# Kernel tuning notes

Hardware: AMD Instinct MI355X
Metric: run time of the kernel (lower is better)

The kernel has to match this reference:

```python
import jax, jax.numpy as jnp
import numpy as np

TEMPERATURE = 0.2
EPS = 1e-10

def setup_inputs() -> dict:
    key = jax.random.key(0)
    x = jax.random.normal(key, (8, 1024, 64, 64), dtype=jnp.float32)
    return {"x": x}

def reference(x):
    B, C, H, W = x.shape
    xf = x.reshape(B, C, H * W)                      # [B, C, HW]
    dot = jnp.einsum('bcn,bdn->bcd', xf, xf) / TEMPERATURE  # [B, C, C]
    logits = jax.nn.softmax(dot, axis=-1)
    diag = jnp.diagonal(logits, axis1=-2, axis2=-1)  # [B, C]
    loss = -jnp.log(diag + EPS)
    return jnp.mean(loss)
```

## Files before the change

### kernel.cpp

```cpp
#include <hip/hip_runtime.h>
#include <hip/hip_bf16.h>

#define BATCH 8
#define CCH 1024
#define NHW 4096
#define SCALE 5.0f
#define ROWS (BATCH * CCH)

typedef unsigned short u16;
typedef __attribute__((ext_vector_type(8))) short short8;
typedef __attribute__((ext_vector_type(4))) float float4v;

__device__ __forceinline__ void async_load16(const void* gsrc, void* ldst) {
    __builtin_amdgcn_global_load_lds(
        (__attribute__((address_space(1))) void*)gsrc,
        (__attribute__((address_space(3))) void*)ldst,
        16, 0, 0);
}

__device__ __forceinline__ u16 f2bf(float f) {
    union { float f; unsigned int u; } c; c.f = f;
    unsigned int u = c.u;
    unsigned int r = u + 0x7FFFu + ((u >> 16) & 1u);
    return (u16)(r >> 16);
}

template <bool CONVERT>
__global__ __launch_bounds__(256) void prep_kernel(const float* __restrict__ x,
                                                   u16* __restrict__ xbf,
                                                   float* __restrict__ diag,
                                                   float* __restrict__ l_acc) {
    const int row = blockIdx.x;
    const int tid = threadIdx.x;
    const float* src = x + (size_t)row * NHW;
    float ssum = 0.f;
#pragma unroll
    for (int p = 0; p < 4; ++p) {
        const int idx = p * 1024 + tid * 4;
        float4 v = *(const float4*)(src + idx);
        ssum += v.x * v.x + v.y * v.y + v.z * v.z + v.w * v.w;
        if (CONVERT) {
            ushort4 o;
            o.x = f2bf(v.x); o.y = f2bf(v.y); o.z = f2bf(v.z); o.w = f2bf(v.w);
            *(ushort4*)(xbf + (size_t)row * NHW + idx) = o;
        }
    }
#pragma unroll
    for (int m = 1; m < 64; m <<= 1) ssum += __shfl_xor(ssum, m);
    __shared__ float red[4];
    if ((tid & 63) == 0) red[tid >> 6] = ssum;
    __syncthreads();
    if (tid == 0) {
        diag[row] = (red[0] + red[1] + red[2] + red[3]) * SCALE;
        l_acc[row] = 0.f;
    }
}

template <bool BF16SRC>
__global__ __launch_bounds__(256) void gram_kernel(const u16* __restrict__ Xbf,
                                                   const float* __restrict__ Xf,
                                                   const float* __restrict__ diag,
                                                   float* __restrict__ l_acc,
                                                   float* __restrict__ num) {
    __shared__ __align__(16) u16 As[8192];
    __shared__ __align__(16) u16 Bs[4096];

    const int bid = blockIdx.x;
    const int b = bid & 7;
    const int t = bid >> 3;

    int bi = 0;
#pragma unroll
    for (int i = 7; i >= 1; --i) {
        if (t >= i * (17 - i)) { bi = i; break; }
    }
    const int bj2 = 2 * bi + (t - bi * (17 - bi));

    const int tid  = threadIdx.x;
    const int lane = tid & 63;
    const int w    = tid >> 6;
    const int wm   = w >> 1;
    const int wn   = w & 1;

    const int st_r  = lane >> 3;
    const int st_kc = (lane & 7) ^ (st_r & 7);

    const u16*   pA  = nullptr; const u16*   pB  = nullptr;
    const float* pAf = nullptr; const float* pBf = nullptr;
    if (BF16SRC) {
        const u16* baseX = Xbf + (size_t)b * CCH * NHW;
        pA = baseX + (size_t)(bi * 128 + w * 32 + st_r) * NHW + st_kc * 8;
        pB = baseX + (size_t)(bj2 * 64 + w * 16 + st_r) * NHW + st_kc * 8;
    } else {
        const float* baseXf = Xf + (size_t)b * CCH * NHW;
        pAf = baseXf + (size_t)(bi * 128 + w * 32 + st_r) * NHW + st_kc * 8;
        pBf = baseXf + (size_t)(bj2 * 64 + w * 16 + st_r) * NHW + st_kc * 8;
    }

    float4v acc[4][2] = {};

    for (int K0 = 0; K0 < NHW; K0 += 64) {
        __syncthreads();
        if (BF16SRC) {
#pragma unroll
            for (int t8 = 0; t8 < 4; ++t8)
                async_load16(pA + (size_t)t8 * 8 * NHW,
                             As + (size_t)(w * 32 + t8 * 8) * 64);
#pragma unroll
            for (int t8 = 0; t8 < 2; ++t8)
                async_load16(pB + (size_t)t8 * 8 * NHW,
                             Bs + (size_t)(w * 16 + t8 * 8) * 64);
            pA += 64; pB += 64;
        } else {
#pragma unroll
            for (int t8 = 0; t8 < 4; ++t8) {
                const float* s = pAf + (size_t)t8 * 8 * NHW;
                float4 f0 = *(const float4*)(s);
                float4 f1 = *(const float4*)(s + 4);
                u16* d = As + (size_t)(w * 32 + t8 * 8 + st_r) * 64 + (lane & 7) * 8;
                d[0]=f2bf(f0.x); d[1]=f2bf(f0.y); d[2]=f2bf(f0.z); d[3]=f2bf(f0.w);
                d[4]=f2bf(f1.x); d[5]=f2bf(f1.y); d[6]=f2bf(f1.z); d[7]=f2bf(f1.w);
            }
#pragma unroll
            for (int t8 = 0; t8 < 2; ++t8) {
                const float* s = pBf + (size_t)t8 * 8 * NHW;
                float4 f0 = *(const float4*)(s);
                float4 f1 = *(const float4*)(s + 4);
                u16* d = Bs + (size_t)(w * 16 + t8 * 8 + st_r) * 64 + (lane & 7) * 8;
                d[0]=f2bf(f0.x); d[1]=f2bf(f0.y); d[2]=f2bf(f0.z); d[3]=f2bf(f0.w);
                d[4]=f2bf(f1.x); d[5]=f2bf(f1.y); d[6]=f2bf(f1.z); d[7]=f2bf(f1.w);
            }
            pAf += 64; pBf += 64;
        }
        __syncthreads();

#pragma unroll
        for (int ks = 0; ks < 2; ++ks) {
            short8 af[4], bf[2];
            const int kq = ks * 4 + (lane >> 4);
            const int rl = lane & 15;
            const int slot = kq ^ (rl & 7);
#pragma unroll
            for (int mt = 0; mt < 4; ++mt)
                af[mt] = *(const short8*)(As + (size_t)(wm * 64 + mt * 16 + rl) * 64 + slot * 8);
#pragma unroll
            for (int nt = 0; nt < 2; ++nt)
                bf[nt] = *(const short8*)(Bs + (size_t)(wn * 32 + nt * 16 + rl) * 64 + slot * 8);
#pragma unroll
            for (int mt = 0; mt < 4; ++mt)
#pragma unroll
                for (int nt = 0; nt < 2; ++nt)
                    acc[mt][nt] = __builtin_amdgcn_mfma_f32_16x16x32_bf16(af[mt], bf[nt], acc[mt][nt], 0, 0, 0);
        }
    }

    const int q  = lane >> 4;
    const int cl = lane & 15;
    const int rowbase = bi * 128 + wm * 64;
    const int colbase = bj2 * 64 + wn * 32;
    const float* dgb = diag + b * CCH;
    float* lb = l_acc + b * CCH;

#pragma unroll
    for (int mt = 0; mt < 4; ++mt) {
#pragma unroll
        for (int reg = 0; reg < 4; ++reg) {
            const int gr = rowbase + mt * 16 + q * 4 + reg;
            const float dg = dgb[gr];
            float s = 0.f;
#pragma unroll
            for (int nt = 0; nt < 2; ++nt) {
                const int gc = colbase + nt * 16 + cl;
                const float e = __expf(acc[mt][nt][reg] * SCALE - dg);
                if (gr <= gc) s += e;
                if (gr == gc) num[b * CCH + gr] = e;
            }
            s += __shfl_xor(s, 1);
            s += __shfl_xor(s, 2);
            s += __shfl_xor(s, 4);
            s += __shfl_xor(s, 8);
            if (cl == 0) atomicAdd(lb + gr, s);
        }
    }

#pragma unroll
    for (int nt = 0; nt < 2; ++nt) {
        const int gc = colbase + nt * 16 + cl;
        const float dgc = dgb[gc];
        float s = 0.f;
#pragma unroll
        for (int mt = 0; mt < 4; ++mt) {
#pragma unroll
            for (int reg = 0; reg < 4; ++reg) {
                const int gr = rowbase + mt * 16 + q * 4 + reg;
                if (gr < gc) s += __expf(acc[mt][nt][reg] * SCALE - dgc);
            }
        }
        s += __shfl_xor(s, 16);
        s += __shfl_xor(s, 32);
        if (lane < 16) atomicAdd(lb + gc, s);
    }
}

__global__ __launch_bounds__(1024) void finalize_kernel(const float* __restrict__ l_acc,
                                                        const float* __restrict__ num,
                                                        float* __restrict__ out) {
    const int tid = threadIdx.x;
    float s = 0.f;
    for (int r = tid; r < ROWS; r += 1024) {
        const float d = num[r] / l_acc[r];
        s += -__logf(d + 1e-10f);
    }
#pragma unroll
    for (int m = 1; m < 64; m <<= 1) s += __shfl_xor(s, m);
    __shared__ float red[16];
    if ((tid & 63) == 0) red[tid >> 6] = s;
    __syncthreads();
    if (tid == 0) {
        float tot = 0.f;
#pragma unroll
        for (int i = 0; i < 16; ++i) tot += red[i];
        out[0] = tot * (1.0f / (float)ROWS);
    }
}

extern "C" void kernel_launch(void* const* d_in, const int* in_sizes, int n_in,
                              void* d_out, int out_size, void* d_ws, size_t ws_size,
                              hipStream_t stream) {
    const float* x = (const float*)d_in[0];
    float* out = (float*)d_out;

    const size_t xbf_bytes  = (size_t)BATCH * CCH * NHW * 2;
    const size_t stat_bytes = (size_t)ROWS * 4;
    const bool fast = ws_size >= xbf_bytes + 3 * stat_bytes;

    const int ntiles = 72;

    if (fast) {
        u16*   xbf   = (u16*)d_ws;
        float* diag  = (float*)((char*)d_ws + xbf_bytes);
        float* l_acc = diag + ROWS;
        float* num   = l_acc + ROWS;
        prep_kernel<true><<<ROWS, 256, 0, stream>>>(x, xbf, diag, l_acc);
        gram_kernel<true><<<BATCH * ntiles, 256, 0, stream>>>(xbf, nullptr, diag, l_acc, num);
        finalize_kernel<<<1, 1024, 0, stream>>>(l_acc, num, out);
    } else {
        float* diag  = (float*)d_ws;
        float* l_acc = diag + ROWS;
        float* num   = l_acc + ROWS;
        prep_kernel<false><<<ROWS, 256, 0, stream>>>(x, nullptr, diag, l_acc);
        gram_kernel<false><<<BATCH * ntiles, 256, 0, stream>>>(nullptr, x, diag, l_acc, num);
        finalize_kernel<<<1, 1024, 0, stream>>>(l_acc, num, out);
    }
}
```

Baseline: 255.7 us.

## Switch Gram kernel to 64x64 upper-triangular tiles with K=128 steps

Replaces the 128x64 block tiling over the symmetric Gram matrix with 64x64 tiles covering the upper triangle (136 tiles per batch instead of 72). Diagonal tiles load only one operand and reuse it as both A and B. The K loop now steps by 128 with a reworked XOR swizzle for LDS. The aim is less wasted work on the diagonal and more blocks for better occupancy across CUs. The cost is lower per-block data reuse and more loads and atomics in total.

```diff
diff --git a/kernel.cpp b/kernel.cpp
--- a/kernel.cpp
+++ b/kernel.cpp
@@ -63,7 +63,7 @@
                                                    float* __restrict__ l_acc,
                                                    float* __restrict__ num) {
     __shared__ __align__(16) u16 As[8192];
-    __shared__ __align__(16) u16 Bs[4096];
+    __shared__ __align__(16) u16 Bs[8192];
 
     const int bid = blockIdx.x;
     const int b = bid & 7;
@@ -71,10 +71,11 @@
 
     int bi = 0;
 #pragma unroll
-    for (int i = 7; i >= 1; --i) {
-        if (t >= i * (17 - i)) { bi = i; break; }
-    }
-    const int bj2 = 2 * bi + (t - bi * (17 - bi));
+    for (int i = 15; i >= 1; --i) {
+        if (t >= i * 16 - (i * (i - 1)) / 2) { bi = i; break; }
+    }
+    const int bj = bi + (t - (bi * 16 - (bi * (bi - 1)) / 2));
+    const bool diagtile = (bi == bj);
 
     const int tid  = threadIdx.x;
     const int lane = tid & 63;
@@ -82,72 +83,82 @@
     const int wm   = w >> 1;
     const int wn   = w & 1;
 
-    const int st_r  = lane >> 3;
-    const int st_kc = (lane & 7) ^ (st_r & 7);
+    const int st_r4 = lane >> 4;
+    const int st_k0 = (lane & 15) ^ st_r4;
 
     const u16*   pA  = nullptr; const u16*   pB  = nullptr;
     const float* pAf = nullptr; const float* pBf = nullptr;
     if (BF16SRC) {
         const u16* baseX = Xbf + (size_t)b * CCH * NHW;
-        pA = baseX + (size_t)(bi * 128 + w * 32 + st_r) * NHW + st_kc * 8;
-        pB = baseX + (size_t)(bj2 * 64 + w * 16 + st_r) * NHW + st_kc * 8;
+        pA = baseX + (size_t)(bi * 64 + w * 16 + st_r4) * NHW;
+        pB = baseX + (size_t)(bj * 64 + w * 16 + st_r4) * NHW;
     } else {
         const float* baseXf = Xf + (size_t)b * CCH * NHW;
-        pAf = baseXf + (size_t)(bi * 128 + w * 32 + st_r) * NHW + st_kc * 8;
-        pBf = baseXf + (size_t)(bj2 * 64 + w * 16 + st_r) * NHW + st_kc * 8;
-    }
-
-    float4v acc[4][2] = {};
-
-    for (int K0 = 0; K0 < NHW; K0 += 64) {
+        pAf = baseXf + (size_t)(bi * 64 + w * 16 + st_r4) * NHW;
+        pBf = baseXf + (size_t)(bj * 64 + w * 16 + st_r4) * NHW;
+    }
+
+    float4v acc[2][2] = {};
+
+    for (int K0 = 0; K0 < NHW; K0 += 128) {
         __syncthreads();
         if (BF16SRC) {
 #pragma unroll
-            for (int t8 = 0; t8 < 4; ++t8)
-                async_load16(pA + (size_t)t8 * 8 * NHW,
-                             As + (size_t)(w * 32 + t8 * 8) * 64);
-#pragma unroll
-            for (int t8 = 0; t8 < 2; ++t8)
-                async_load16(pB + (size_t)t8 * 8 * NHW,
-                             Bs + (size_t)(w * 16 + t8 * 8) * 64);
-            pA += 64; pB += 64;
+            for (int t4 = 0; t4 < 4; ++t4) {
+                const int kc = st_k0 ^ (t4 * 4);
+                async_load16(pA + (size_t)(t4 * 4) * NHW + K0 + kc * 8,
+                             As + (size_t)(w * 16 + t4 * 4) * 128);
+            }
+            if (!diagtile) {
+#pragma unroll
+                for (int t4 = 0; t4 < 4; ++t4) {
+                    const int kc = st_k0 ^ (t4 * 4);
+                    async_load16(pB + (size_t)(t4 * 4) * NHW + K0 + kc * 8,
+                                 Bs + (size_t)(w * 16 + t4 * 4) * 128);
+                }
+            }
         } else {
 #pragma unroll
-            for (int t8 = 0; t8 < 4; ++t8) {
-                const float* s = pAf + (size_t)t8 * 8 * NHW;
+            for (int t4 = 0; t4 < 4; ++t4) {
+                const int kc = st_k0 ^ (t4 * 4);
+                const float* s = pAf + (size_t)(t4 * 4) * NHW + K0 + kc * 8;
                 float4 f0 = *(const float4*)(s);
                 float4 f1 = *(const float4*)(s + 4);
-                u16* d = As + (size_t)(w * 32 + t8 * 8 + st_r) * 64 + (lane & 7) * 8;
+                u16* d = As + (size_t)(w * 16 + t4 * 4 + st_r4) * 128 + (lane & 15) * 8;
                 d[0]=f2bf(f0.x); d[1]=f2bf(f0.y); d[2]=f2bf(f0.z); d[3]=f2bf(f0.w);
                 d[4]=f2bf(f1.x); d[5]=f2bf(f1.y); d[6]=f2bf(f1.z); d[7]=f2bf(f1.w);
             }
-#pragma unroll
-            for (int t8 = 0; t8 < 2; ++t8) {
-                const float* s = pBf + (size_t)t8 * 8 * NHW;
-                float4 f0 = *(const float4*)(s);
-                float4 f1 = *(const float4*)(s + 4);
-                u16* d = Bs + (size_t)(w * 16 + t8 * 8 + st_r) * 64 + (lane & 7) * 8;
-                d[0]=f2bf(f0.x); d[1]=f2bf(f0.y); d[2]=f2bf(f0.z); d[3]=f2bf(f0.w);
-                d[4]=f2bf(f1.x); d[5]=f2bf(f1.y); d[6]=f2bf(f1.z); d[7]=f2bf(f1.w);
-            }
-            pAf += 64; pBf += 64;
+            if (!diagtile) {
+#pragma unroll
+                for (int t4 = 0; t4 < 4; ++t4) {
+                    const int kc = st_k0 ^ (t4 * 4);
+                    const float* s = pBf + (size_t)(t4 * 4) * NHW + K0 + kc * 8;
+                    float4 f0 = *(const float4*)(s);
+                    float4 f1 = *(const float4*)(s + 4);
+                    u16* d = Bs + (size_t)(w * 16 + t4 * 4 + st_r4) * 128 + (lane & 15) * 8;
+                    d[0]=f2bf(f0.x); d[1]=f2bf(f0.y); d[2]=f2bf(f0.z); d[3]=f2bf(f0.w);
+                    d[4]=f2bf(f1.x); d[5]=f2bf(f1.y); d[6]=f2bf(f1.z); d[7]=f2bf(f1.w);
+                }
+            }
         }
         __syncthreads();
 
-#pragma unroll
-        for (int ks = 0; ks < 2; ++ks) {
-            short8 af[4], bf[2];
-            const int kq = ks * 4 + (lane >> 4);
+        const u16* Bbase = diagtile ? As : Bs;
+#pragma unroll
+        for (int ks = 0; ks < 4; ++ks) {
+            short8 af[2], bf[2];
+            const int q  = lane >> 4;
             const int rl = lane & 15;
-            const int slot = kq ^ (rl & 7);
-#pragma unroll
-            for (int mt = 0; mt < 4; ++mt)
-                af[mt] = *(const short8*)(As + (size_t)(wm * 64 + mt * 16 + rl) * 64 + slot * 8);
+            const int kq = ks * 4 + q;
+            const int slot = kq ^ rl;
+#pragma unroll
+            for (int mt = 0; mt < 2; ++mt)
+                af[mt] = *(const short8*)(As + (size_t)(wm * 32 + mt * 16 + rl) * 128 + slot * 8);
 #pragma unroll
             for (int nt = 0; nt < 2; ++nt)
-                bf[nt] = *(const short8*)(Bs + (size_t)(wn * 32 + nt * 16 + rl) * 64 + slot * 8);
-#pragma unroll
-            for (int mt = 0; mt < 4; ++mt)
+                bf[nt] = *(const short8*)(Bbase + (size_t)(wn * 32 + nt * 16 + rl) * 128 + slot * 8);
+#pragma unroll
+            for (int mt = 0; mt < 2; ++mt)
 #pragma unroll
                 for (int nt = 0; nt < 2; ++nt)
                     acc[mt][nt] = __builtin_amdgcn_mfma_f32_16x16x32_bf16(af[mt], bf[nt], acc[mt][nt], 0, 0, 0);
@@ -156,13 +167,13 @@
 
     const int q  = lane >> 4;
     const int cl = lane & 15;
-    const int rowbase = bi * 128 + wm * 64;
-    const int colbase = bj2 * 64 + wn * 32;
+    const int rowbase = bi * 64 + wm * 32;
+    const int colbase = bj * 64 + wn * 32;
     const float* dgb = diag + b * CCH;
     float* lb = l_acc + b * CCH;
 
 #pragma unroll
-    for (int mt = 0; mt < 4; ++mt) {
+    for (int mt = 0; mt < 2; ++mt) {
 #pragma unroll
         for (int reg = 0; reg < 4; ++reg) {
             const int gr = rowbase + mt * 16 + q * 4 + reg;
@@ -189,7 +200,7 @@
         const float dgc = dgb[gc];
         float s = 0.f;
 #pragma unroll
-        for (int mt = 0; mt < 4; ++mt) {
+        for (int mt = 0; mt < 2; ++mt) {
 #pragma unroll
             for (int reg = 0; reg < 4; ++reg) {
                 const int gr = rowbase + mt * 16 + q * 4 + reg;
@@ -234,7 +245,7 @@
     const size_t stat_bytes = (size_t)ROWS * 4;
     const bool fast = ws_size >= xbf_bytes + 3 * stat_bytes;
 
-    const int ntiles = 72;
+    const int ntiles = 136;
 
     if (fast) {
         u16*   xbf   = (u16*)d_ws;
```

Result: slower. 263.1 us (+2.9%).

## Switch Gram matrix path from bf16 to fp8 MFMA with diagonal tile aliasing

Applied to the files above, without the earlier changes.

Quantizes the input to fp8 instead of bf16 in the prep pass, halving the workspace footprint, and runs the Gram matrix on the fp8 16x16x32 MFMA with a K step of 128 per LDS stage. The diagonal is computed from the dequantized fp8 values so it matches the off-diagonal products. Diagonal tiles, where the B block lies inside the A block, skip the B load and read B from the A buffer. This cuts global and LDS traffic and doubles matrix throughput, at the cost of much lower precision in logits scaled by 5.

```diff
diff --git a/kernel.cpp b/kernel.cpp
--- a/kernel.cpp
+++ b/kernel.cpp
@@ -7,8 +7,8 @@
 #define SCALE 5.0f
 #define ROWS (BATCH * CCH)
 
-typedef unsigned short u16;
-typedef __attribute__((ext_vector_type(8))) short short8;
+typedef unsigned char u8;
+typedef unsigned int u32;
 typedef __attribute__((ext_vector_type(4))) float float4v;
 
 __device__ __forceinline__ void async_load16(const void* gsrc, void* ldst) {
@@ -18,16 +18,23 @@
         16, 0, 0);
 }
 
-__device__ __forceinline__ u16 f2bf(float f) {
-    union { float f; unsigned int u; } c; c.f = f;
-    unsigned int u = c.u;
-    unsigned int r = u + 0x7FFFu + ((u >> 16) & 1u);
-    return (u16)(r >> 16);
+__device__ __forceinline__ u32 pk4_fp8(float a, float b, float c, float d) {
+    u32 v = __builtin_amdgcn_cvt_pk_fp8_f32(a, b, 0, false);
+    v = __builtin_amdgcn_cvt_pk_fp8_f32(c, d, v, true);
+    return v;
+}
+
+__device__ __forceinline__ float ssq4_fp8(u32 q) {
+    float d0 = __builtin_amdgcn_cvt_f32_fp8(q, 0);
+    float d1 = __builtin_amdgcn_cvt_f32_fp8(q, 1);
+    float d2 = __builtin_amdgcn_cvt_f32_fp8(q, 2);
+    float d3 = __builtin_amdgcn_cvt_f32_fp8(q, 3);
+    return d0 * d0 + d1 * d1 + d2 * d2 + d3 * d3;
 }
 
 template <bool CONVERT>
 __global__ __launch_bounds__(256) void prep_kernel(const float* __restrict__ x,
-                                                   u16* __restrict__ xbf,
+                                                   u8* __restrict__ xq,
                                                    float* __restrict__ diag,
                                                    float* __restrict__ l_acc) {
     const int row = blockIdx.x;
@@ -38,12 +45,9 @@
     for (int p = 0; p < 4; ++p) {
         const int idx = p * 1024 + tid * 4;
         float4 v = *(const float4*)(src + idx);
-        ssum += v.x * v.x + v.y * v.y + v.z * v.z + v.w * v.w;
-        if (CONVERT) {
-            ushort4 o;
-            o.x = f2bf(v.x); o.y = f2bf(v.y); o.z = f2bf(v.z); o.w = f2bf(v.w);
-            *(ushort4*)(xbf + (size_t)row * NHW + idx) = o;
-        }
+        const u32 q = pk4_fp8(v.x, v.y, v.z, v.w);
+        ssum += ssq4_fp8(q);
+        if (CONVERT) *(u32*)(xq + (size_t)row * NHW + idx) = q;
     }
 #pragma unroll
     for (int m = 1; m < 64; m <<= 1) ssum += __shfl_xor(ssum, m);
@@ -56,14 +60,14 @@
     }
 }
 
-template <bool BF16SRC>
-__global__ __launch_bounds__(256) void gram_kernel(const u16* __restrict__ Xbf,
+template <bool QSRC>
+__global__ __launch_bounds__(256) void gram_kernel(const u8* __restrict__ Xq,
                                                    const float* __restrict__ Xf,
                                                    const float* __restrict__ diag,
                                                    float* __restrict__ l_acc,
                                                    float* __restrict__ num) {
-    __shared__ __align__(16) u16 As[8192];
-    __shared__ __align__(16) u16 Bs[4096];
+    __shared__ __align__(16) u8 As[16384];
+    __shared__ __align__(16) u8 Bs[8192];
 
     const int bid = blockIdx.x;
     const int b = bid & 7;
@@ -75,6 +79,7 @@
         if (t >= i * (17 - i)) { bi = i; break; }
     }
     const int bj2 = 2 * bi + (t - bi * (17 - bi));
+    const bool aliasB = (bj2 == 2 * bi) || (bj2 == 2 * bi + 1);
 
     const int tid  = threadIdx.x;
     const int lane = tid & 63;
@@ -83,74 +88,88 @@
     const int wn   = w & 1;
 
     const int st_r  = lane >> 3;
-    const int st_kc = (lane & 7) ^ (st_r & 7);
-
-    const u16*   pA  = nullptr; const u16*   pB  = nullptr;
+    const int st_kc = (lane & 7) ^ st_r;
+
+    const u8*    pA  = nullptr; const u8*    pB  = nullptr;
     const float* pAf = nullptr; const float* pBf = nullptr;
-    if (BF16SRC) {
-        const u16* baseX = Xbf + (size_t)b * CCH * NHW;
-        pA = baseX + (size_t)(bi * 128 + w * 32 + st_r) * NHW + st_kc * 8;
-        pB = baseX + (size_t)(bj2 * 64 + w * 16 + st_r) * NHW + st_kc * 8;
+    if (QSRC) {
+        const u8* baseX = Xq + (size_t)b * CCH * NHW;
+        pA = baseX + (size_t)(bi * 128 + w * 32 + st_r) * NHW + st_kc * 16;
+        pB = baseX + (size_t)(bj2 * 64 + w * 16 + st_r) * NHW + st_kc * 16;
     } else {
         const float* baseXf = Xf + (size_t)b * CCH * NHW;
-        pAf = baseXf + (size_t)(bi * 128 + w * 32 + st_r) * NHW + st_kc * 8;
-        pBf = baseXf + (size_t)(bj2 * 64 + w * 16 + st_r) * NHW + st_kc * 8;
+        pAf = baseXf + (size_t)(bi * 128 + w * 32 + st_r) * NHW + st_kc * 16;
+        pBf = baseXf + (size_t)(bj2 * 64 + w * 16 + st_r) * NHW + st_kc * 16;
     }
 
     float4v acc[4][2] = {};
 
-    for (int K0 = 0; K0 < NHW; K0 += 64) {
+    for (int K0 = 0; K0 < NHW; K0 += 128) {
         __syncthreads();
-        if (BF16SRC) {
+        if (QSRC) {
 #pragma unroll
             for (int t8 = 0; t8 < 4; ++t8)
-                async_load16(pA + (size_t)t8 * 8 * NHW,
-                             As + (size_t)(w * 32 + t8 * 8) * 64);
-#pragma unroll
-            for (int t8 = 0; t8 < 2; ++t8)
-                async_load16(pB + (size_t)t8 * 8 * NHW,
-                             Bs + (size_t)(w * 16 + t8 * 8) * 64);
-            pA += 64; pB += 64;
+                async_load16(pA + (size_t)(t8 * 8) * NHW + K0,
+                             As + (size_t)(w * 32 + t8 * 8) * 128);
+            if (!aliasB) {
+#pragma unroll
+                for (int t8 = 0; t8 < 2; ++t8)
+                    async_load16(pB + (size_t)(t8 * 8) * NHW + K0,
+                                 Bs + (size_t)(w * 16 + t8 * 8) * 128);
+            }
         } else {
 #pragma unroll
             for (int t8 = 0; t8 < 4; ++t8) {
-                const float* s = pAf + (size_t)t8 * 8 * NHW;
+                const float* s = pAf + (size_t)(t8 * 8) * NHW + K0;
                 float4 f0 = *(const float4*)(s);
                 float4 f1 = *(const float4*)(s + 4);
-                u16* d = As + (size_t)(w * 32 + t8 * 8 + st_r) * 64 + (lane & 7) * 8;
-                d[0]=f2bf(f0.x); d[1]=f2bf(f0.y); d[2]=f2bf(f0.z); d[3]=f2bf(f0.w);
-                d[4]=f2bf(f1.x); d[5]=f2bf(f1.y); d[6]=f2bf(f1.z); d[7]=f2bf(f1.w);
-            }
-#pragma unroll
-            for (int t8 = 0; t8 < 2; ++t8) {
-                const float* s = pBf + (size_t)t8 * 8 * NHW;
-                float4 f0 = *(const float4*)(s);
-                float4 f1 = *(const float4*)(s + 4);
-                u16* d = Bs + (size_t)(w * 16 + t8 * 8 + st_r) * 64 + (lane & 7) * 8;
-                d[0]=f2bf(f0.x); d[1]=f2bf(f0.y); d[2]=f2bf(f0.z); d[3]=f2bf(f0.w);
-                d[4]=f2bf(f1.x); d[5]=f2bf(f1.y); d[6]=f2bf(f1.z); d[7]=f2bf(f1.w);
-            }
-            pAf += 64; pBf += 64;
+                float4 f2 = *(const float4*)(s + 8);
+                float4 f3 = *(const float4*)(s + 12);
+                u32* d = (u32*)(As + (size_t)(w * 32 + t8 * 8 + st_r) * 128 + (lane & 7) * 16);
+                d[0] = pk4_fp8(f0.x, f0.y, f0.z, f0.w);
+                d[1] = pk4_fp8(f1.x, f1.y, f1.z, f1.w);
+                d[2] = pk4_fp8(f2.x, f2.y, f2.z, f2.w);
+                d[3] = pk4_fp8(f3.x, f3.y, f3.z, f3.w);
+            }
+            if (!aliasB) {
+#pragma unroll
+                for (int t8 = 0; t8 < 2; ++t8) {
+                    const float* s = pBf + (size_t)(t8 * 8) * NHW + K0;
+                    float4 f0 = *(const float4*)(s);
+                    float4 f1 = *(const float4*)(s + 4);
+                    float4 f2 = *(const float4*)(s + 8);
+                    float4 f3 = *(const float4*)(s + 12);
+                    u32* d = (u32*)(Bs + (size_t)(w * 16 + t8 * 8 + st_r) * 128 + (lane & 7) * 16);
+                    d[0] = pk4_fp8(f0.x, f0.y, f0.z, f0.w);
+                    d[1] = pk4_fp8(f1.x, f1.y, f1.z, f1.w);
+                    d[2] = pk4_fp8(f2.x, f2.y, f2.z, f2.w);
+                    d[3] = pk4_fp8(f3.x, f3.y, f3.z, f3.w);
+                }
+            }
         }
         __syncthreads();
 
-#pragma unroll
-        for (int ks = 0; ks < 2; ++ks) {
-            short8 af[4], bf[2];
-            const int kq = ks * 4 + (lane >> 4);
-            const int rl = lane & 15;
-            const int slot = kq ^ (rl & 7);
+        const u8* Bbase = aliasB ? (As + (size_t)(bj2 - 2 * bi) * 64 * 128) : Bs;
+        const int q  = lane >> 4;
+        const int rl = lane & 15;
+#pragma unroll
+        for (int s = 0; s < 4; ++s) {
+            const int cbase = 2 * s + (q >> 1);
+            const int off8  = (q & 1) * 8;
+            long af[4], bf[2];
 #pragma unroll
             for (int mt = 0; mt < 4; ++mt)
-                af[mt] = *(const short8*)(As + (size_t)(wm * 64 + mt * 16 + rl) * 64 + slot * 8);
+                af[mt] = *(const long*)(As + (size_t)(wm * 64 + mt * 16 + rl) * 128
+                                           + (size_t)(cbase ^ (rl & 7)) * 16 + off8);
 #pragma unroll
             for (int nt = 0; nt < 2; ++nt)
-                bf[nt] = *(const short8*)(Bs + (size_t)(wn * 32 + nt * 16 + rl) * 64 + slot * 8);
+                bf[nt] = *(const long*)(Bbase + (size_t)(wn * 32 + nt * 16 + rl) * 128
+                                              + (size_t)(cbase ^ (rl & 7)) * 16 + off8);
 #pragma unroll
             for (int mt = 0; mt < 4; ++mt)
 #pragma unroll
                 for (int nt = 0; nt < 2; ++nt)
-                    acc[mt][nt] = __builtin_amdgcn_mfma_f32_16x16x32_bf16(af[mt], bf[nt], acc[mt][nt], 0, 0, 0);
+                    acc[mt][nt] = __builtin_amdgcn_mfma_f32_16x16x32_fp8_fp8(af[mt], bf[nt], acc[mt][nt], 0, 0, 0);
         }
     }
 
@@ -230,19 +249,19 @@
     const float* x = (const float*)d_in[0];
     float* out = (float*)d_out;
 
-    const size_t xbf_bytes  = (size_t)BATCH * CCH * NHW * 2;
+    const size_t xq_bytes   = (size_t)BATCH * CCH * NHW;
     const size_t stat_bytes = (size_t)ROWS * 4;
-    const bool fast = ws_size >= xbf_bytes + 3 * stat_bytes;
+    const bool fast = ws_size >= xq_bytes + 3 * stat_bytes;
 
     const int ntiles = 72;
 
     if (fast) {
-        u16*   xbf   = (u16*)d_ws;
-        float* diag  = (float*)((char*)d_ws + xbf_bytes);
+        u8*    xq    = (u8*)d_ws;
+        float* diag  = (float*)((char*)d_ws + xq_bytes);
         float* l_acc = diag + ROWS;
         float* num   = l_acc + ROWS;
-        prep_kernel<true><<<ROWS, 256, 0, stream>>>(x, xbf, diag, l_acc);
-        gram_kernel<true><<<BATCH * ntiles, 256, 0, stream>>>(xbf, nullptr, diag, l_acc, num);
+        prep_kernel<true><<<ROWS, 256, 0, stream>>>(x, xq, diag, l_acc);
+        gram_kernel<true><<<BATCH * ntiles, 256, 0, stream>>>(xq, nullptr, diag, l_acc, num);
         finalize_kernel<<<1, 1024, 0, stream>>>(l_acc, num, out);
     } else {
         float* diag  = (float*)d_ws;
```

Result: faster. 243.1 us (-4.9%).
